# Optimization experiments

Measured on AMD Instinct MI355X. Metric: run time of the kernel, lower is better.

Reference implementation:

```python
import jax, jax.numpy as jnp
import numpy as np

T, B, E, H = 2048, 2, 1024, 16
Dh = E // H


def setup_inputs() -> dict:
    key = jax.random.key(0)
    ks = jax.random.split(key, 5)
    s = 0.02
    query = jax.random.normal(ks[0], (T, B, E), dtype=jnp.float32)
    Wq = jax.random.normal(ks[1], (E, E), dtype=jnp.float32) * s
    Wk = jax.random.normal(ks[2], (E, E), dtype=jnp.float32) * s
    Wv = jax.random.normal(ks[3], (E, E), dtype=jnp.float32) * s
    Wo = jax.random.normal(ks[4], (E, E), dtype=jnp.float32) * s
    bq = jnp.zeros((E,), jnp.float32)
    bk = jnp.zeros((E,), jnp.float32)
    bv = jnp.zeros((E,), jnp.float32)
    bo = jnp.zeros((E,), jnp.float32)
    # additive causal mask: 0 on/below diagonal, -inf above (standard fairseq usage)
    neg = jnp.finfo(jnp.float32).min
    attn_mask = jnp.where(jnp.triu(jnp.ones((T, T), jnp.bool_), k=1), neg, 0.0).astype(jnp.float32)
    return {"query": query, "Wq": Wq, "bq": bq, "Wk": Wk, "bk": bk,
            "Wv": Wv, "bv": bv, "Wo": Wo, "bo": bo, "attn_mask": attn_mask}


def reference(query, Wq, bq, Wk, bk, Wv, bv, Wo, bo, attn_mask):
    t, b, e = query.shape
    scale = Dh ** -0.5
    # self-attention projections (nn.Linear: x @ W.T + b)
    q = (query @ Wq.T + bq) * scale  # [T,B,E]
    k = query @ Wk.T + bk
    v = query @ Wv.T + bv
    # [T, B*H, Dh] -> [B*H, T, Dh]
    q = q.reshape(t, b * H, Dh).transpose(1, 0, 2)
    k = k.reshape(t, b * H, Dh).transpose(1, 0, 2)
    v = v.reshape(t, b * H, Dh).transpose(1, 0, 2)
    # explicit bmm -> softmax -> bmm (materializes [B*H, T, T])
    attn_weights = jnp.einsum('btd,bsd->bts', q, k) + attn_mask[None, :, :]
    attn_probs = jax.nn.softmax(attn_weights, axis=-1)
    attn = jnp.einsum('bts,bsd->btd', attn_probs, v)  # [B*H, T, Dh]
    attn = attn.transpose(1, 0, 2).reshape(t, b, e)  # [T,B,E]
    out = attn @ Wo.T + bo
    return out
```

## Files before the change

kernel.cpp:

```cpp
#include <hip/hip_runtime.h>


typedef __attribute__((ext_vector_type(8))) short   s16x8;
typedef __attribute__((ext_vector_type(4))) float   f32x4;
typedef __attribute__((ext_vector_type(2))) __fp16  f16x2;
typedef __attribute__((ext_vector_type(4))) __fp16  f16x4;

#define MFMA16(a, b, c) __builtin_amdgcn_mfma_f32_16x16x32_bf16((a), (b), (c), 0, 0, 0)
#define MFMApv(a, b, c) __builtin_amdgcn_mfma_f32_16x16x16f16((a), (b), (c), 0, 0, 0)

static __device__ __forceinline__ unsigned short f2bf(float f) {
    unsigned u = __float_as_uint(f);
    unsigned r = u + 0x7fffu + ((u >> 16) & 1u);
    return (unsigned short)(r >> 16);
}

static __device__ __forceinline__ void gl2lds16(const void* g, void* l) {
    __builtin_amdgcn_global_load_lds(
        (const __attribute__((address_space(1))) unsigned int*)g,
        (__attribute__((address_space(3))) unsigned int*)l, 16, 0, 0);
}

__global__ __launch_bounds__(256) void cvt_all(const float* __restrict__ query,
                                               const float* __restrict__ w0,
                                               const float* __restrict__ w1,
                                               const float* __restrict__ w2,
                                               const float* __restrict__ w3,
                                               unsigned short* __restrict__ Xb,
                                               unsigned short* __restrict__ Wcat) {
    const int bx = blockIdx.x;
    if (bx < 4096) {
        const int i = threadIdx.x;
        const float4 f = reinterpret_cast<const float4*>(query + (size_t)bx * 1024)[i];
        ushort4 u;
        u.x = f2bf(f.x); u.y = f2bf(f.y); u.z = f2bf(f.z); u.w = f2bf(f.w);
        const int mrow = (bx & 1) * 2048 + (bx >> 1);
        reinterpret_cast<ushort4*>(Xb + (size_t)mrow * 1024)[i] = u;
    } else {
        const int j   = bx - 4096;
        const int sel = j >> 10;
        const int i   = (j & 1023) * 256 + threadIdx.x;
        const float* src = (sel == 0) ? w0 : (sel == 1) ? w1 : (sel == 2) ? w2 : w3;
        const float4 f = reinterpret_cast<const float4*>(src)[i];
        ushort4 u;
        u.x = f2bf(f.x); u.y = f2bf(f.y); u.z = f2bf(f.z); u.w = f2bf(f.w);
        reinterpret_cast<ushort4*>(Wcat + (size_t)sel * 1048576)[i] = u;
    }
}

__global__ __launch_bounds__(512, 2) void gemm_qkv(const unsigned short* __restrict__ A,
                                                   const unsigned short* __restrict__ W,
                                                   const float* __restrict__ b0,
                                                   const float* __restrict__ b1,
                                                   const float* __restrict__ b2,
                                                   unsigned short* __restrict__ outQK,
                                                   __fp16* __restrict__ outV) {
    __shared__ __align__(16) unsigned short smem[57344];

    const int tid  = threadIdx.x;
    const int w    = tid >> 6;
    const int lane = tid & 63;
    const int quad = lane >> 4;
    const int c    = lane & 15;
    const int wm   = w >> 2;
    const int wn   = w & 3;

    const int id   = blockIdx.x;
    const int xcd  = id & 7;
    const int slot = id >> 3;
    const int m0 = (xcd * 2 + (slot & 1)) * 256;
    const int n0 = (slot >> 1) * 192;

    f32x4 acc[8][3];
    #pragma unroll
    for (int mi = 0; mi < 8; ++mi)
        #pragma unroll
        for (int ni = 0; ni < 3; ++ni) acc[mi][ni] = (f32x4){0.f, 0.f, 0.f, 0.f};

    const int srow = tid >> 3;
    const int g    = (tid & 7) ^ (srow & 7);
    const unsigned short* aG = A + (size_t)(m0 + srow) * 1024 + g * 8;
    const unsigned short* wG = W + (size_t)(n0 + srow) * 1024 + g * 8;
    const int loff = tid * 8;

#define STA(buf, u, k0) gl2lds16(aG + (k0) + (u) * 65536, &smem[(buf) * 28672 + (u) * 4096 + loff])
#define STB(buf, u, k0) gl2lds16(wG + (k0) + (u) * 65536, &smem[(buf) * 28672 + 16384 + (u) * 4096 + loff])

    STB(0, 0, 0); STB(0, 1, 0); STB(0, 2, 0);
    STA(0, 0, 0); STA(0, 2, 0); STA(0, 1, 0); STA(0, 3, 0);
    asm volatile("s_waitcnt vmcnt(2)" ::: "memory");
    asm volatile("s_barrier" ::: "memory");

    const int cs  = c & 7;
    const int ch0 = (quad ^ cs) << 3;
    const int ch1 = ((4 + quad) ^ cs) << 3;

    s16x8 af[4][2], bf[3][2];

    #pragma unroll
    for (int mi = 0; mi < 4; ++mi) {
        const int row = (wm * 128 + mi * 16 + c) * 64;
        af[mi][0] = *reinterpret_cast<const s16x8*>(&smem[row + ch0]);
        af[mi][1] = *reinterpret_cast<const s16x8*>(&smem[row + ch1]);
    }
    #pragma unroll
    for (int ni = 0; ni < 3; ++ni) {
        const int row = (wn * 48 + ni * 16 + c) * 64;
        bf[ni][0] = *reinterpret_cast<const s16x8*>(&smem[16384 + row + ch0]);
        bf[ni][1] = *reinterpret_cast<const s16x8*>(&smem[16384 + row + ch1]);
    }

    #pragma unroll 1
    for (int t = 0; t < 16; ++t) {
        const unsigned short* Al = &smem[(t & 1) * 28672];
        const int  nb   = (t & 1) ^ 1;
        const int  kn   = (t + 1) * 64;
        const bool more = (t < 15);

        if (more) {
            STB(nb, 0, kn); STB(nb, 1, kn); STB(nb, 2, kn);
            STA(nb, 0, kn); STA(nb, 2, kn); STA(nb, 1, kn); STA(nb, 3, kn);
        }

        __builtin_amdgcn_s_setprio(1);
        #pragma unroll
        for (int mi = 0; mi < 4; ++mi)
            #pragma unroll
            for (int ni = 0; ni < 3; ++ni) {
                acc[mi][ni] = MFMA16(af[mi][0], bf[ni][0], acc[mi][ni]);
                acc[mi][ni] = MFMA16(af[mi][1], bf[ni][1], acc[mi][ni]);
            }
        __builtin_amdgcn_s_setprio(0);

        if (more) asm volatile("s_waitcnt vmcnt(7)" ::: "memory");
        else      asm volatile("s_waitcnt vmcnt(0)" ::: "memory");
        asm volatile("s_barrier" ::: "memory");

        #pragma unroll
        for (int mi = 0; mi < 4; ++mi) {
            const int row = (wm * 128 + 64 + mi * 16 + c) * 64;
            af[mi][0] = *reinterpret_cast<const s16x8*>(&Al[row + ch0]);
            af[mi][1] = *reinterpret_cast<const s16x8*>(&Al[row + ch1]);
        }
        __builtin_amdgcn_s_setprio(1);
        #pragma unroll
        for (int mi = 0; mi < 4; ++mi)
            #pragma unroll
            for (int ni = 0; ni < 3; ++ni) {
                acc[4 + mi][ni] = MFMA16(af[mi][0], bf[ni][0], acc[4 + mi][ni]);
                acc[4 + mi][ni] = MFMA16(af[mi][1], bf[ni][1], acc[4 + mi][ni]);
            }
        __builtin_amdgcn_s_setprio(0);

        if (more) {
            asm volatile("s_waitcnt vmcnt(2)" ::: "memory");
            asm volatile("s_barrier" ::: "memory");
            const unsigned short* An = &smem[nb * 28672];
            #pragma unroll
            for (int mi = 0; mi < 4; ++mi) {
                const int row = (wm * 128 + mi * 16 + c) * 64;
                af[mi][0] = *reinterpret_cast<const s16x8*>(&An[row + ch0]);
                af[mi][1] = *reinterpret_cast<const s16x8*>(&An[row + ch1]);
            }
            #pragma unroll
            for (int ni = 0; ni < 3; ++ni) {
                const int row = (wn * 48 + ni * 16 + c) * 64;
                bf[ni][0] = *reinterpret_cast<const s16x8*>(&An[16384 + row + ch0]);
                bf[ni][1] = *reinterpret_cast<const s16x8*>(&An[16384 + row + ch1]);
            }
        }
    }
#undef STA
#undef STB

    const float qs = 0.18033688011112042f;
    #pragma unroll
    for (int ni = 0; ni < 3; ++ni) {
        const int n = n0 + wn * 48 + ni * 16 + c;
        if (n < 2048) {
            const float bval  = (n < 1024) ? b0[n] : b1[n & 1023];
            const float scale = (n < 1024) ? qs : 1.0f;
            #pragma unroll
            for (int mi = 0; mi < 8; ++mi)
                #pragma unroll
                for (int r = 0; r < 4; ++r) {
                    const int m = m0 + wm * 128 + mi * 16 + quad * 4 + r;
                    outQK[(size_t)m * 2048 + n] = f2bf((acc[mi][ni][r] + bval) * scale);
                }
        }
    }

    if (n0 >= 1920) {
        const int vg0 = (n0 >= 2048) ? (n0 - 2048) : 0;
        const int nV  = n0 + 192 - ((n0 > 2048) ? n0 : 2048);
        __fp16* lds16 = reinterpret_cast<__fp16*>(smem);
        __syncthreads();
        #pragma unroll
        for (int ni = 0; ni < 3; ++ni) {
            const int n = n0 + wn * 48 + ni * 16 + c;
            if (n >= 2048) {
                const int lv = (n - 2048) - vg0;
                const float bval = b2[n - 2048];
                #pragma unroll
                for (int mi = 0; mi < 8; ++mi) {
                    const int m = wm * 128 + mi * 16 + quad * 4;
                    const f16x2 lo = __builtin_amdgcn_cvt_pkrtz(acc[mi][ni][0] + bval,
                                                                acc[mi][ni][1] + bval);
                    const f16x2 hi = __builtin_amdgcn_cvt_pkrtz(acc[mi][ni][2] + bval,
                                                                acc[mi][ni][3] + bval);
                    uint2 st;
                    st.x = __builtin_bit_cast(unsigned int, lo);
                    st.y = __builtin_bit_cast(unsigned int, hi);
                    const int phys = lv * 256 + (((m >> 3) ^ (lv & 31)) << 3) + (m & 7);
                    *reinterpret_cast<uint2*>(&lds16[phys]) = st;
                }
            }
        }
        __syncthreads();
        const int lv = tid >> 1;
        if (lv < nV) {
            const int vcol = vg0 + lv;
            const int bb = m0 >> 11, tbase = m0 & 2047;
            __fp16* vdst = outV + ((size_t)((bb * 16 + (vcol >> 6)) * 64 + (vcol & 63))) * 2048 + tbase;
            #pragma unroll
            for (int j = 0; j < 16; ++j) {
                const int lc = (tid & 1) * 16 + j;
                *reinterpret_cast<uint4*>(vdst + lc * 8) =
                    *reinterpret_cast<const uint4*>(&lds16[lv * 256 + ((lc ^ (lv & 31)) << 3)]);
            }
        }
    }
}

__global__ __launch_bounds__(256) void gemm_out(const unsigned short* __restrict__ A,
                                                const unsigned short* __restrict__ W,
                                                const float* __restrict__ bias,
                                                float* __restrict__ outF) {
    __shared__ __align__(16) unsigned short Al[2][64 * 64];
    __shared__ __align__(16) unsigned short Bl[2][128 * 64];

    const int tid  = threadIdx.x;
    const int w    = tid >> 6;
    const int lane = tid & 63;
    const int quad = lane >> 4;
    const int c    = lane & 15;

    const int id   = blockIdx.x;
    const int xcd  = id & 7;
    const int slot = id >> 3;
    const int m0 = (xcd * 8 + (slot & 7)) * 64;
    const int n0 = (slot >> 3) * 128;

    f32x4 acc[8];
    #pragma unroll
    for (int ni = 0; ni < 8; ++ni) acc[ni] = (f32x4){0.f, 0.f, 0.f, 0.f};

    const int srow = tid >> 3;
    const int g    = (tid & 7) ^ (srow & 7);
    const unsigned short* aG = A + (size_t)(m0 + srow) * 1024 + g * 8;
    const unsigned short* wG = W + (size_t)(n0 + srow) * 1024 + g * 8;
    const int loff = tid * 8;

    const int cs = (c & 7);

    gl2lds16(aG,             &Al[0][loff]);
    gl2lds16(aG + 32 * 1024, &Al[0][loff + 2048]);
    #pragma unroll
    for (int i = 0; i < 4; ++i)
        gl2lds16(wG + i * 32 * 1024, &Bl[0][loff + i * 2048]);

    #pragma unroll 1
    for (int kk = 0; kk < 16; ++kk) {
        __syncthreads();
        if (kk < 15) {
            const int k0n = (kk + 1) * 64;
            const int nb  = (kk + 1) & 1;
            gl2lds16(aG + k0n,             &Al[nb][loff]);
            gl2lds16(aG + k0n + 32 * 1024, &Al[nb][loff + 2048]);
            #pragma unroll
            for (int i = 0; i < 4; ++i)
                gl2lds16(wG + k0n + i * 32 * 1024, &Bl[nb][loff + i * 2048]);
        }
        const int cb = kk & 1;
        const int arow = (w * 16 + c) * 64;
        const s16x8 af0 = *reinterpret_cast<const s16x8*>(&Al[cb][arow + ((quad ^ cs) << 3)]);
        const s16x8 af1 = *reinterpret_cast<const s16x8*>(&Al[cb][arow + (((4 + quad) ^ cs) << 3)]);
        __builtin_amdgcn_s_setprio(1);
        #pragma unroll
        for (int ni = 0; ni < 8; ++ni) {
            const int brow = (ni * 16 + c) * 64;
            const s16x8 bf0 = *reinterpret_cast<const s16x8*>(&Bl[cb][brow + ((quad ^ cs) << 3)]);
            const s16x8 bf1 = *reinterpret_cast<const s16x8*>(&Bl[cb][brow + (((4 + quad) ^ cs) << 3)]);
            acc[ni] = MFMA16(af0, bf0, acc[ni]);
            acc[ni] = MFMA16(af1, bf1, acc[ni]);
        }
        __builtin_amdgcn_s_setprio(0);
    }

    #pragma unroll
    for (int ni = 0; ni < 8; ++ni) {
        const int n = n0 + ni * 16 + c;
        const float bval = bias[n];
        const int m = m0 + w * 16 + quad * 4;
        const int bb = m >> 11, t = m & 2047;
        #pragma unroll
        for (int r = 0; r < 4; ++r)
            outF[(size_t)(2 * (t + r) + bb) * 1024 + n] = acc[ni][r] + bval;
    }
}

__global__ __launch_bounds__(256, 2) void attn_kernel(const unsigned short* __restrict__ QKb,
                                                      const __fp16* __restrict__ Vt,
                                                      unsigned short* __restrict__ Ob) {
    __shared__ unsigned short Kl[2][2][64][32];
    __shared__ __fp16 Vl[2][64][64];

    const int tid  = threadIdx.x;
    const int w    = tid >> 6;
    const int lane = tid & 63;
    const int quad = lane >> 4;
    const int c    = lane & 15;

    const int id = blockIdx.x;
    const int bh = (id & 7) * 4 + ((id >> 3) & 3);
    const int kidx = id >> 5;
    const int a    = (kidx < 8) ? (15 - kidx) : (kidx - 8);
    const int bB = bh >> 4, h = bh & 15;
    const int t0 = a * 128;
    const int trg = t0 + w * 32;
    const int nIt = 2 * a + 2;

    const unsigned short* qp0 = QKb + (size_t)(bB * 2048 + trg + c) * 2048 + h * 64 + quad * 8;
    const s16x8 aq0 = *reinterpret_cast<const s16x8*>(qp0);
    const s16x8 aq1 = *reinterpret_cast<const s16x8*>(qp0 + 32);
    const unsigned short* qp1 = qp0 + (size_t)16 * 2048;
    const s16x8 aq2 = *reinterpret_cast<const s16x8*>(qp1);
    const s16x8 aq3 = *reinterpret_cast<const s16x8*>(qp1 + 32);

    const int lr4 = lane >> 2, sl4 = lane & 3;
    const unsigned short* kSrc = QKb + (size_t)(bB * 2048 + w * 16 + lr4) * 2048
                                 + 1024 + h * 64 + (sl4 ^ ((lane >> 3) & 3)) * 8;
    const int vr8 = lane >> 3, sl8 = lane & 7;
    const __fp16* vSrcA = Vt + (size_t)(bh * 64 + w * 16 + vr8) * 2048 + (sl8 ^ vr8) * 8;
    const __fp16* vSrcB = vSrcA + (size_t)8 * 2048;

    f32x4 acc0[4], acc1[4];
    float l0 = 0.f, l1 = 0.f;
    #pragma unroll
    for (int dt = 0; dt < 4; ++dt) {
        acc0[dt] = (f32x4){0.f, 0.f, 0.f, 0.f};
        acc1[dt] = (f32x4){0.f, 0.f, 0.f, 0.f};
    }

    const int kswz = (quad ^ ((c >> 1) & 3)) * 8;

    {
        gl2lds16(kSrc,      &Kl[0][0][w * 16 + lr4][sl4 * 8]);
        gl2lds16(kSrc + 32, &Kl[0][1][w * 16 + lr4][sl4 * 8]);
        gl2lds16(vSrcA,     &Vl[0][w * 16 + vr8][sl8 * 8]);
        gl2lds16(vSrcB,     &Vl[0][w * 16 + 8 + vr8][sl8 * 8]);
    }

    for (int it = 0; it < nIt; ++it) {
        const int buf = it & 1;
        __syncthreads();
        if (it + 1 < nIt) {
            const size_t s1 = (size_t)(it + 1) * 64;
            const int nb = buf ^ 1;
            gl2lds16(kSrc + s1 * 2048,      &Kl[nb][0][w * 16 + lr4][sl4 * 8]);
            gl2lds16(kSrc + s1 * 2048 + 32, &Kl[nb][1][w * 16 + lr4][sl4 * 8]);
            gl2lds16(vSrcA + s1,            &Vl[nb][w * 16 + vr8][sl8 * 8]);
            gl2lds16(vSrcB + s1,            &Vl[nb][w * 16 + 8 + vr8][sl8 * 8]);
        }

        s16x8 kf[4][2];
        #pragma unroll
        for (int ns = 0; ns < 4; ++ns) {
            kf[ns][0] = *reinterpret_cast<const s16x8*>(&Kl[buf][0][ns * 16 + c][kswz]);
            kf[ns][1] = *reinterpret_cast<const s16x8*>(&Kl[buf][1][ns * 16 + c][kswz]);
        }
        f16x4 vf[4][4];
        #pragma unroll
        for (int dt = 0; dt < 4; ++dt)
            #pragma unroll
            for (int ch = 0; ch < 4; ++ch) {
                const int phys = ((2 * ch + (quad >> 1)) ^ (c & 7)) * 8 + (quad & 1) * 4;
                vf[dt][ch] = *reinterpret_cast<const f16x4*>(&Vl[buf][dt * 16 + c][phys]);
            }

        const int s0 = it * 64;

        f32x4 sT[4];
        __builtin_amdgcn_s_setprio(1);
        #pragma unroll
        for (int ns = 0; ns < 4; ++ns) {
            f32x4 z = (f32x4){0.f, 0.f, 0.f, 0.f};
            z = MFMA16(kf[ns][0], aq0, z);
            sT[ns] = MFMA16(kf[ns][1], aq1, z);
        }
        __builtin_amdgcn_s_setprio(0);
        f16x4 pf0[4];
        {
            const bool dg = (s0 + 63 > trg);
            float lp = 0.f;
            #pragma unroll
            for (int ns = 0; ns < 4; ++ns) {
                float pv[4];
                #pragma unroll
                for (int r = 0; r < 4; ++r) pv[r] = __builtin_amdgcn_exp2f(sT[ns][r]);
                if (dg) {
                    const int sb = s0 + ns * 16 + quad * 4;
                    const int qg = trg + c;
                    #pragma unroll
                    for (int r = 0; r < 4; ++r) if (sb + r > qg) pv[r] = 0.f;
                }
                lp += (pv[0] + pv[1]) + (pv[2] + pv[3]);
                const f16x2 lo = __builtin_amdgcn_cvt_pkrtz(pv[0], pv[1]);
                const f16x2 hi = __builtin_amdgcn_cvt_pkrtz(pv[2], pv[3]);
                pf0[ns] = __builtin_shufflevector(lo, hi, 0, 1, 2, 3);
            }
            l0 += lp;
        }

        __builtin_amdgcn_s_setprio(1);
        #pragma unroll
        for (int ns = 0; ns < 4; ++ns) {
            f32x4 z = (f32x4){0.f, 0.f, 0.f, 0.f};
            z = MFMA16(kf[ns][0], aq2, z);
            sT[ns] = MFMA16(kf[ns][1], aq3, z);
        }
        __builtin_amdgcn_s_setprio(0);
        f16x4 pf1[4];
        {
            const bool dg = (s0 + 63 > trg + 16);
            float lp = 0.f;
            #pragma unroll
            for (int ns = 0; ns < 4; ++ns) {
                float pv[4];
                #pragma unroll
                for (int r = 0; r < 4; ++r) pv[r] = __builtin_amdgcn_exp2f(sT[ns][r]);
                if (dg) {
                    const int sb = s0 + ns * 16 + quad * 4;
                    const int qg = trg + 16 + c;
                    #pragma unroll
                    for (int r = 0; r < 4; ++r) if (sb + r > qg) pv[r] = 0.f;
                }
                lp += (pv[0] + pv[1]) + (pv[2] + pv[3]);
                const f16x2 lo = __builtin_amdgcn_cvt_pkrtz(pv[0], pv[1]);
                const f16x2 hi = __builtin_amdgcn_cvt_pkrtz(pv[2], pv[3]);
                pf1[ns] = __builtin_shufflevector(lo, hi, 0, 1, 2, 3);
            }
            l1 += lp;
        }

        __builtin_amdgcn_s_setprio(1);
        #pragma unroll
        for (int dt = 0; dt < 4; ++dt)
            #pragma unroll
            for (int ns = 0; ns < 4; ++ns) {
                acc0[dt] = MFMApv(vf[dt][ns], pf0[ns], acc0[dt]);
                acc1[dt] = MFMApv(vf[dt][ns], pf1[ns], acc1[dt]);
            }
        __builtin_amdgcn_s_setprio(0);
    }

    float lv0 = l0;
    lv0 += __shfl_xor(lv0, 16);
    lv0 += __shfl_xor(lv0, 32);
    const float inv0 = 1.0f / lv0;
    float lv1 = l1;
    lv1 += __shfl_xor(lv1, 16);
    lv1 += __shfl_xor(lv1, 32);
    const float inv1 = 1.0f / lv1;

    const size_t base0 = (size_t)(bB * 2048 + trg + c) * 1024 + h * 64;
    const size_t base1 = base0 + (size_t)16 * 1024;
    #pragma unroll
    for (int dt = 0; dt < 4; ++dt) {
        unsigned u0 = (unsigned)f2bf(acc0[dt][0] * inv0)
                    | ((unsigned)f2bf(acc0[dt][1] * inv0) << 16);
        unsigned u1 = (unsigned)f2bf(acc0[dt][2] * inv0)
                    | ((unsigned)f2bf(acc0[dt][3] * inv0) << 16);
        uint2 st; st.x = u0; st.y = u1;
        *reinterpret_cast<uint2*>(Ob + base0 + dt * 16 + quad * 4) = st;
        u0 = (unsigned)f2bf(acc1[dt][0] * inv1)
           | ((unsigned)f2bf(acc1[dt][1] * inv1) << 16);
        u1 = (unsigned)f2bf(acc1[dt][2] * inv1)
           | ((unsigned)f2bf(acc1[dt][3] * inv1) << 16);
        uint2 st2; st2.x = u0; st2.y = u1;
        *reinterpret_cast<uint2*>(Ob + base1 + dt * 16 + quad * 4) = st2;
    }
}

extern "C" void kernel_launch(void* const* d_in, const int* in_sizes, int n_in,
                              void* d_out, int out_size, void* d_ws, size_t ws_size,
                              hipStream_t stream) {
    const float* query = (const float*)d_in[0];
    const float* Wq    = (const float*)d_in[1];
    const float* bq    = (const float*)d_in[2];
    const float* Wk    = (const float*)d_in[3];
    const float* bk    = (const float*)d_in[4];
    const float* Wv    = (const float*)d_in[5];
    const float* bv    = (const float*)d_in[6];
    const float* Wo    = (const float*)d_in[7];
    const float* bo    = (const float*)d_in[8];

    float* out = (float*)d_out;

    unsigned short* ws    = (unsigned short*)d_ws;
    unsigned short* Xbf   = ws;
    unsigned short* Wcat  = Xbf  + (size_t)4096 * 1024;
    unsigned short* QKb   = Wcat + (size_t)4 * 1024 * 1024;
    __fp16*         Vtw   = (__fp16*)(QKb + (size_t)4096 * 2048);
    unsigned short* attnb = (unsigned short*)(Vtw + (size_t)32 * 64 * 2048);

    cvt_all<<<8192, 256, 0, stream>>>(query, Wq, Wk, Wv, Wo, Xbf, Wcat);

    gemm_qkv<<<256, 512, 0, stream>>>(Xbf, Wcat, bq, bk, bv, QKb, Vtw);

    attn_kernel<<<512, 256, 0, stream>>>(QKb, Vtw, attnb);

    gemm_out<<<512, 256, 0, stream>>>(attnb, Wcat + (size_t)3 * 1024 * 1024,
                                      bo, out);
}
```

Before: 205.6 us.

## Split causal attention rows into KV chunks with combine pass; widen QKV GEMM tiles

```diff
diff --git a/kernel.cpp b/kernel.cpp
--- a/kernel.cpp
+++ b/kernel.cpp
@@ -55,7 +55,7 @@
                                                    const float* __restrict__ b2,
                                                    unsigned short* __restrict__ outQK,
                                                    __fp16* __restrict__ outV) {
-    __shared__ __align__(16) unsigned short smem[57344];
+    __shared__ __align__(16) unsigned short smem[65536];
 
     const int tid  = threadIdx.x;
     const int w    = tid >> 6;
@@ -69,13 +69,13 @@
     const int xcd  = id & 7;
     const int slot = id >> 3;
     const int m0 = (xcd * 2 + (slot & 1)) * 256;
-    const int n0 = (slot >> 1) * 192;
-
-    f32x4 acc[8][3];
+    const int n0 = (slot >> 1) * 256;
+
+    f32x4 acc[8][4];
     #pragma unroll
     for (int mi = 0; mi < 8; ++mi)
         #pragma unroll
-        for (int ni = 0; ni < 3; ++ni) acc[mi][ni] = (f32x4){0.f, 0.f, 0.f, 0.f};
+        for (int ni = 0; ni < 4; ++ni) acc[mi][ni] = (f32x4){0.f, 0.f, 0.f, 0.f};
 
     const int srow = tid >> 3;
     const int g    = (tid & 7) ^ (srow & 7);
@@ -83,10 +83,10 @@
     const unsigned short* wG = W + (size_t)(n0 + srow) * 1024 + g * 8;
     const int loff = tid * 8;
 
-#define STA(buf, u, k0) gl2lds16(aG + (k0) + (u) * 65536, &smem[(buf) * 28672 + (u) * 4096 + loff])
-#define STB(buf, u, k0) gl2lds16(wG + (k0) + (u) * 65536, &smem[(buf) * 28672 + 16384 + (u) * 4096 + loff])
-
-    STB(0, 0, 0); STB(0, 1, 0); STB(0, 2, 0);
+#define STA(buf, u, k0) gl2lds16(aG + (k0) + (u) * 65536, &smem[(buf) * 32768 + (u) * 4096 + loff])
+#define STB(buf, u, k0) gl2lds16(wG + (k0) + (u) * 65536, &smem[(buf) * 32768 + 16384 + (u) * 4096 + loff])
+
+    STB(0, 0, 0); STB(0, 1, 0); STB(0, 2, 0); STB(0, 3, 0);
     STA(0, 0, 0); STA(0, 2, 0); STA(0, 1, 0); STA(0, 3, 0);
     asm volatile("s_waitcnt vmcnt(2)" ::: "memory");
     asm volatile("s_barrier" ::: "memory");
@@ -95,7 +95,7 @@
     const int ch0 = (quad ^ cs) << 3;
     const int ch1 = ((4 + quad) ^ cs) << 3;
 
-    s16x8 af[4][2], bf[3][2];
+    s16x8 af[4][2], bf[4][2];
 
     #pragma unroll
     for (int mi = 0; mi < 4; ++mi) {
@@ -104,21 +104,21 @@
         af[mi][1] = *reinterpret_cast<const s16x8*>(&smem[row + ch1]);
     }
     #pragma unroll
-    for (int ni = 0; ni < 3; ++ni) {
-        const int row = (wn * 48 + ni * 16 + c) * 64;
+    for (int ni = 0; ni < 4; ++ni) {
+        const int row = (wn * 64 + ni * 16 + c) * 64;
         bf[ni][0] = *reinterpret_cast<const s16x8*>(&smem[16384 + row + ch0]);
         bf[ni][1] = *reinterpret_cast<const s16x8*>(&smem[16384 + row + ch1]);
     }
 
     #pragma unroll 1
     for (int t = 0; t < 16; ++t) {
-        const unsigned short* Al = &smem[(t & 1) * 28672];
+        const unsigned short* Al = &smem[(t & 1) * 32768];
         const int  nb   = (t & 1) ^ 1;
         const int  kn   = (t + 1) * 64;
         const bool more = (t < 15);
 
         if (more) {
-            STB(nb, 0, kn); STB(nb, 1, kn); STB(nb, 2, kn);
+            STB(nb, 0, kn); STB(nb, 1, kn); STB(nb, 2, kn); STB(nb, 3, kn);
             STA(nb, 0, kn); STA(nb, 2, kn); STA(nb, 1, kn); STA(nb, 3, kn);
         }
 
@@ -126,13 +126,13 @@
         #pragma unroll
         for (int mi = 0; mi < 4; ++mi)
             #pragma unroll
-            for (int ni = 0; ni < 3; ++ni) {
+            for (int ni = 0; ni < 4; ++ni) {
                 acc[mi][ni] = MFMA16(af[mi][0], bf[ni][0], acc[mi][ni]);
                 acc[mi][ni] = MFMA16(af[mi][1], bf[ni][1], acc[mi][ni]);
             }
         __builtin_amdgcn_s_setprio(0);
 
-        if (more) asm volatile("s_waitcnt vmcnt(7)" ::: "memory");
+        if (more) asm volatile("s_waitcnt vmcnt(8)" ::: "memory");
         else      asm volatile("s_waitcnt vmcnt(0)" ::: "memory");
         asm volatile("s_barrier" ::: "memory");
 
@@ -146,7 +146,7 @@
         #pragma unroll
         for (int mi = 0; mi < 4; ++mi)
             #pragma unroll
-            for (int ni = 0; ni < 3; ++ni) {
+            for (int ni = 0; ni < 4; ++ni) {
                 acc[4 + mi][ni] = MFMA16(af[mi][0], bf[ni][0], acc[4 + mi][ni]);
                 acc[4 + mi][ni] = MFMA16(af[mi][1], bf[ni][1], acc[4 + mi][ni]);
             }
@@ -155,7 +155,7 @@
         if (more) {
             asm volatile("s_waitcnt vmcnt(2)" ::: "memory");
             asm volatile("s_barrier" ::: "memory");
-            const unsigned short* An = &smem[nb * 28672];
+            const unsigned short* An = &smem[nb * 32768];
             #pragma unroll
             for (int mi = 0; mi < 4; ++mi) {
                 const int row = (wm * 128 + mi * 16 + c) * 64;
@@ -163,8 +163,8 @@
                 af[mi][1] = *reinterpret_cast<const s16x8*>(&An[row + ch1]);
             }
             #pragma unroll
-            for (int ni = 0; ni < 3; ++ni) {
-                const int row = (wn * 48 + ni * 16 + c) * 64;
+            for (int ni = 0; ni < 4; ++ni) {
+                const int row = (wn * 64 + ni * 16 + c) * 64;
                 bf[ni][0] = *reinterpret_cast<const s16x8*>(&An[16384 + row + ch0]);
                 bf[ni][1] = *reinterpret_cast<const s16x8*>(&An[16384 + row + ch1]);
             }
@@ -173,13 +173,13 @@
 #undef STA
 #undef STB
 
-    const float qs = 0.18033688011112042f;
-    #pragma unroll
-    for (int ni = 0; ni < 3; ++ni) {
-        const int n = n0 + wn * 48 + ni * 16 + c;
-        if (n < 2048) {
-            const float bval  = (n < 1024) ? b0[n] : b1[n & 1023];
-            const float scale = (n < 1024) ? qs : 1.0f;
+    if (n0 < 2048) {
+        const float scale = (n0 < 1024) ? 0.18033688011112042f : 1.0f;
+        const float* bias = (n0 < 1024) ? b0 : b1;
+        #pragma unroll
+        for (int ni = 0; ni < 4; ++ni) {
+            const int n = n0 + wn * 64 + ni * 16 + c;
+            const float bval = bias[n & 1023];
             #pragma unroll
             for (int mi = 0; mi < 8; ++mi)
                 #pragma unroll
@@ -188,45 +188,46 @@
                     outQK[(size_t)m * 2048 + n] = f2bf((acc[mi][ni][r] + bval) * scale);
                 }
         }
-    }
-
-    if (n0 >= 1920) {
-        const int vg0 = (n0 >= 2048) ? (n0 - 2048) : 0;
-        const int nV  = n0 + 192 - ((n0 > 2048) ? n0 : 2048);
+    } else {
         __fp16* lds16 = reinterpret_cast<__fp16*>(smem);
-        __syncthreads();
-        #pragma unroll
-        for (int ni = 0; ni < 3; ++ni) {
-            const int n = n0 + wn * 48 + ni * 16 + c;
-            if (n >= 2048) {
-                const int lv = (n - 2048) - vg0;
-                const float bval = b2[n - 2048];
+        #pragma unroll 1
+        for (int tn = 0; tn < 2; ++tn) {
+            __syncthreads();
+            if ((wn >> 1) == tn) {
                 #pragma unroll
-                for (int mi = 0; mi < 8; ++mi) {
-                    const int m = wm * 128 + mi * 16 + quad * 4;
-                    const f16x2 lo = __builtin_amdgcn_cvt_pkrtz(acc[mi][ni][0] + bval,
-                                                                acc[mi][ni][1] + bval);
-                    const f16x2 hi = __builtin_amdgcn_cvt_pkrtz(acc[mi][ni][2] + bval,
-                                                                acc[mi][ni][3] + bval);
-                    uint2 st;
-                    st.x = __builtin_bit_cast(unsigned int, lo);
-                    st.y = __builtin_bit_cast(unsigned int, hi);
-                    const int phys = lv * 256 + (((m >> 3) ^ (lv & 31)) << 3) + (m & 7);
-                    *reinterpret_cast<uint2*>(&lds16[phys]) = st;
+                for (int ni = 0; ni < 4; ++ni) {
+                    const int nLoc = (wn & 1) * 64 + ni * 16 + c;
+                    const float bval = b2[(n0 - 2048) + tn * 128 + nLoc];
+                    #pragma unroll
+                    for (int mi = 0; mi < 8; ++mi) {
+                        const int mLoc = mi * 16 + quad * 4;
+                        const f16x2 lo = __builtin_amdgcn_cvt_pkrtz(acc[mi][ni][0] + bval,
+                                                                    acc[mi][ni][1] + bval);
+                        const f16x2 hi = __builtin_amdgcn_cvt_pkrtz(acc[mi][ni][2] + bval,
+                                                                    acc[mi][ni][3] + bval);
+                        uint2 st;
+                        st.x = __builtin_bit_cast(unsigned int, lo);
+                        st.y = __builtin_bit_cast(unsigned int, hi);
+                        const int phys = wm * 16384 + nLoc * 128 +
+                                         (((mLoc >> 3) ^ (nLoc & 15)) << 3) + (mLoc & 7);
+                        *reinterpret_cast<uint2*>(&lds16[phys]) = st;
+                    }
                 }
             }
-        }
-        __syncthreads();
-        const int lv = tid >> 1;
-        if (lv < nV) {
-            const int vcol = vg0 + lv;
-            const int bb = m0 >> 11, tbase = m0 & 2047;
+            __syncthreads();
+            const int np   = tid >> 1;
+            const int rg   = np >> 7;
+            const int nLoc = np & 127;
+            const int vcol = (n0 - 2048) + tn * 128 + nLoc;
+            const int bb = m0 >> 11;
+            const int tbase = (m0 & 2047) + rg * 128;
             __fp16* vdst = outV + ((size_t)((bb * 16 + (vcol >> 6)) * 64 + (vcol & 63))) * 2048 + tbase;
             #pragma unroll
-            for (int j = 0; j < 16; ++j) {
-                const int lc = (tid & 1) * 16 + j;
+            for (int j = 0; j < 8; ++j) {
+                const int lc = (tid & 1) * 8 + j;
                 *reinterpret_cast<uint4*>(vdst + lc * 8) =
-                    *reinterpret_cast<const uint4*>(&lds16[lv * 256 + ((lc ^ (lv & 31)) << 3)]);
+                    *reinterpret_cast<const uint4*>(
+                        &lds16[rg * 16384 + nLoc * 128 + ((lc ^ (nLoc & 15)) << 3)]);
             }
         }
     }
@@ -309,9 +310,11 @@
     }
 }
 
-__global__ __launch_bounds__(256, 2) void attn_kernel(const unsigned short* __restrict__ QKb,
+__global__ __launch_bounds__(256, 4) void attn_kernel(const unsigned short* __restrict__ QKb,
                                                       const __fp16* __restrict__ Vt,
-                                                      unsigned short* __restrict__ Ob) {
+                                                      unsigned short* __restrict__ Ob,
+                                                      float* __restrict__ Po,
+                                                      float* __restrict__ Pl) {
     __shared__ unsigned short Kl[2][2][64][32];
     __shared__ __fp16 Vl[2][64][64];
 
@@ -323,12 +326,22 @@
 
     const int id = blockIdx.x;
     const int bh = (id & 7) * 4 + ((id >> 3) & 3);
-    const int kidx = id >> 5;
-    const int a    = (kidx < 8) ? (15 - kidx) : (kidx - 8);
+    const int e  = 39 - (id >> 5);
+    int a8, ci, nc;
+    if (e < 4)       { a8 = e;               ci = 0;         nc = 1; }
+    else if (e < 12) { const int k = e - 4;  a8 = 4 + (k >> 1); ci = k & 1;     nc = 2; }
+    else if (e < 24) { const int k = e - 12; const int q3 = (k * 11) >> 5;
+                       a8 = 8 + q3;          ci = k - 3 * q3; nc = 3; }
+    else             { const int k = e - 24; a8 = 12 + (k >> 2); ci = k & 3;    nc = 4; }
+    const int U = 2 * a8 + 2;
+    int u0, u1;
+    if (nc == 1)      { u0 = 0;                  u1 = U; }
+    else if (nc == 2) { u0 = (ci * U) >> 1;      u1 = ((ci + 1) * U) >> 1; }
+    else if (nc == 3) { u0 = (ci * U * 11) >> 5; u1 = ((ci + 1) * U * 11) >> 5; }
+    else              { u0 = (ci * U) >> 2;      u1 = ((ci + 1) * U) >> 2; }
+
     const int bB = bh >> 4, h = bh & 15;
-    const int t0 = a * 128;
-    const int trg = t0 + w * 32;
-    const int nIt = 2 * a + 2;
+    const int trg = a8 * 128 + w * 32;
 
     const unsigned short* qp0 = QKb + (size_t)(bB * 2048 + trg + c) * 2048 + h * 64 + quad * 8;
     const s16x8 aq0 = *reinterpret_cast<const s16x8*>(qp0);
@@ -355,16 +368,18 @@
     const int kswz = (quad ^ ((c >> 1) & 3)) * 8;
 
     {
-        gl2lds16(kSrc,      &Kl[0][0][w * 16 + lr4][sl4 * 8]);
-        gl2lds16(kSrc + 32, &Kl[0][1][w * 16 + lr4][sl4 * 8]);
-        gl2lds16(vSrcA,     &Vl[0][w * 16 + vr8][sl8 * 8]);
-        gl2lds16(vSrcB,     &Vl[0][w * 16 + 8 + vr8][sl8 * 8]);
-    }
-
-    for (int it = 0; it < nIt; ++it) {
+        const size_t s0r = (size_t)u0 * 64;
+        const int b0 = u0 & 1;
+        gl2lds16(kSrc + s0r * 2048,      &Kl[b0][0][w * 16 + lr4][sl4 * 8]);
+        gl2lds16(kSrc + s0r * 2048 + 32, &Kl[b0][1][w * 16 + lr4][sl4 * 8]);
+        gl2lds16(vSrcA + s0r,            &Vl[b0][w * 16 + vr8][sl8 * 8]);
+        gl2lds16(vSrcB + s0r,            &Vl[b0][w * 16 + 8 + vr8][sl8 * 8]);
+    }
+
+    for (int it = u0; it < u1; ++it) {
         const int buf = it & 1;
         __syncthreads();
-        if (it + 1 < nIt) {
+        if (it + 1 < u1) {
             const size_t s1 = (size_t)(it + 1) * 64;
             const int nb = buf ^ 1;
             gl2lds16(kSrc + s1 * 2048,      &Kl[nb][0][w * 16 + lr4][sl4 * 8]);
@@ -467,28 +482,91 @@
     float lv0 = l0;
     lv0 += __shfl_xor(lv0, 16);
     lv0 += __shfl_xor(lv0, 32);
-    const float inv0 = 1.0f / lv0;
     float lv1 = l1;
     lv1 += __shfl_xor(lv1, 16);
     lv1 += __shfl_xor(lv1, 32);
-    const float inv1 = 1.0f / lv1;
-
-    const size_t base0 = (size_t)(bB * 2048 + trg + c) * 1024 + h * 64;
-    const size_t base1 = base0 + (size_t)16 * 1024;
-    #pragma unroll
-    for (int dt = 0; dt < 4; ++dt) {
-        unsigned u0 = (unsigned)f2bf(acc0[dt][0] * inv0)
-                    | ((unsigned)f2bf(acc0[dt][1] * inv0) << 16);
-        unsigned u1 = (unsigned)f2bf(acc0[dt][2] * inv0)
-                    | ((unsigned)f2bf(acc0[dt][3] * inv0) << 16);
-        uint2 st; st.x = u0; st.y = u1;
-        *reinterpret_cast<uint2*>(Ob + base0 + dt * 16 + quad * 4) = st;
-        u0 = (unsigned)f2bf(acc1[dt][0] * inv1)
-           | ((unsigned)f2bf(acc1[dt][1] * inv1) << 16);
-        u1 = (unsigned)f2bf(acc1[dt][2] * inv1)
-           | ((unsigned)f2bf(acc1[dt][3] * inv1) << 16);
-        uint2 st2; st2.x = u0; st2.y = u1;
-        *reinterpret_cast<uint2*>(Ob + base1 + dt * 16 + quad * 4) = st2;
+
+    if (nc == 1) {
+        const float inv0 = 1.0f / lv0;
+        const float inv1 = 1.0f / lv1;
+        const size_t base0 = (size_t)(bB * 2048 + trg + c) * 1024 + h * 64;
+        const size_t base1 = base0 + (size_t)16 * 1024;
+        #pragma unroll
+        for (int dt = 0; dt < 4; ++dt) {
+            unsigned x0 = (unsigned)f2bf(acc0[dt][0] * inv0)
+                        | ((unsigned)f2bf(acc0[dt][1] * inv0) << 16);
+            unsigned x1 = (unsigned)f2bf(acc0[dt][2] * inv0)
+                        | ((unsigned)f2bf(acc0[dt][3] * inv0) << 16);
+            uint2 st; st.x = x0; st.y = x1;
+            *reinterpret_cast<uint2*>(Ob + base0 + dt * 16 + quad * 4) = st;
+            x0 = (unsigned)f2bf(acc1[dt][0] * inv1)
+               | ((unsigned)f2bf(acc1[dt][1] * inv1) << 16);
+            x1 = (unsigned)f2bf(acc1[dt][2] * inv1)
+               | ((unsigned)f2bf(acc1[dt][3] * inv1) << 16);
+            uint2 st2; st2.x = x0; st2.y = x1;
+            *reinterpret_cast<uint2*>(Ob + base1 + dt * 16 + quad * 4) = st2;
+        }
+    } else {
+        const int slot = (bh * 16 + a8) * 4 + ci;
+        float* po0 = Po + (size_t)slot * 8192 + (w * 32 + c) * 64 + quad * 4;
+        float* po1 = po0 + 16 * 64;
+        #pragma unroll
+        for (int dt = 0; dt < 4; ++dt) {
+            float4 st;
+            st.x = acc0[dt][0]; st.y = acc0[dt][1]; st.z = acc0[dt][2]; st.w = acc0[dt][3];
+            *reinterpret_cast<float4*>(po0 + dt * 16) = st;
+            float4 st2;
+            st2.x = acc1[dt][0]; st2.y = acc1[dt][1]; st2.z = acc1[dt][2]; st2.w = acc1[dt][3];
+            *reinterpret_cast<float4*>(po1 + dt * 16) = st2;
+        }
+        if (quad == 0) {
+            Pl[(size_t)slot * 128 + w * 32 + c]      = lv0;
+            Pl[(size_t)slot * 128 + w * 32 + 16 + c] = lv1;
+        }
+    }
+}
+
+__global__ __launch_bounds__(256) void attn_combine(const float* __restrict__ Po,
+                                                    const float* __restrict__ Pl,
+                                                    unsigned short* __restrict__ Ob) {
+    const int id   = blockIdx.x;
+    const int bh   = id & 31;
+    const int rest = id >> 5;
+    const int a8   = 4 + (rest >> 1);
+    const int half = rest & 1;
+    const int nc   = (a8 < 8) ? 2 : (a8 < 12) ? 3 : 4;
+    const int bB = bh >> 4, h = bh & 15;
+
+    const int tid = threadIdx.x;
+    const int q   = tid >> 2;
+    const int ds  = (tid & 3) * 16;
+    const int row = half * 64 + q;
+
+    const int slot0 = (bh * 16 + a8) * 4;
+
+    float lsum = 0.f;
+    for (int ci = 0; ci < nc; ++ci) lsum += Pl[(size_t)(slot0 + ci) * 128 + row];
+    const float inv = 1.0f / lsum;
+
+    float4 o[4];
+    #pragma unroll
+    for (int j = 0; j < 4; ++j) o[j] = (float4){0.f, 0.f, 0.f, 0.f};
+    for (int ci = 0; ci < nc; ++ci) {
+        const float* p = Po + (size_t)(slot0 + ci) * 8192 + row * 64 + ds;
+        #pragma unroll
+        for (int j = 0; j < 4; ++j) {
+            const float4 v = reinterpret_cast<const float4*>(p)[j];
+            o[j].x += v.x; o[j].y += v.y; o[j].z += v.z; o[j].w += v.w;
+        }
+    }
+
+    unsigned short* dst = Ob + (size_t)(bB * 2048 + a8 * 128 + row) * 1024 + h * 64 + ds;
+    #pragma unroll
+    for (int j = 0; j < 4; ++j) {
+        uint2 st;
+        st.x = (unsigned)f2bf(o[j].x * inv) | ((unsigned)f2bf(o[j].y * inv) << 16);
+        st.y = (unsigned)f2bf(o[j].z * inv) | ((unsigned)f2bf(o[j].w * inv) << 16);
+        *reinterpret_cast<uint2*>(dst + j * 4) = st;
     }
 }
 
@@ -513,12 +591,16 @@
     unsigned short* QKb   = Wcat + (size_t)4 * 1024 * 1024;
     __fp16*         Vtw   = (__fp16*)(QKb + (size_t)4096 * 2048);
     unsigned short* attnb = (unsigned short*)(Vtw + (size_t)32 * 64 * 2048);
+    float*          Pob   = (float*)(attnb + (size_t)4096 * 1024);
+    float*          Plb   = Pob + (size_t)4096 * 4096;
 
     cvt_all<<<8192, 256, 0, stream>>>(query, Wq, Wk, Wv, Wo, Xbf, Wcat);
 
-    gemm_qkv<<<256, 512, 0, stream>>>(Xbf, Wcat, bq, bk, bv, QKb, Vtw);
-
-    attn_kernel<<<512, 256, 0, stream>>>(QKb, Vtw, attnb);
+    gemm_qkv<<<192, 512, 0, stream>>>(Xbf, Wcat, bq, bk, bv, QKb, Vtw);
+
+    attn_kernel<<<1280, 256, 0, stream>>>(QKb, Vtw, attnb, Pob, Plb);
+
+    attn_combine<<<768, 256, 0, stream>>>(Pob, Plb, attnb);
 
     gemm_out<<<512, 256, 0, stream>>>(attnb, Wcat + (size_t)3 * 1024 * 1024,
                                       bo, out);
```

New measurement: 287.9 us. +40.0%, slower.
